# Optimization experiments

Hardware: AMD Instinct MI355X
Metric: run time of the kernel (lower is better)

The kernel has to match this reference:

```python
import jax, jax.numpy as jnp
import numpy as np
from jax import lax

NMS_RADIUS = 4
THRESHOLD = 0.005
BORDER = 4
MAX_KP = 1024


def _max_pool(x, r):
    # torch max_pool2d pads with -inf; reduce_window 'SAME' pads with init value.
    w = 2 * r + 1
    return lax.reduce_window(x, -jnp.inf, lax.max, (1, w, w), (1, 1, 1), 'SAME')


def simple_nms(scores, radius):
    zeros = jnp.zeros_like(scores)
    max_mask = scores == _max_pool(scores, radius)
    for _ in range(2):
        supp_mask = _max_pool(max_mask.astype(scores.dtype), radius) > 0
        supp_scores = jnp.where(supp_mask, zeros, scores)
        new_max_mask = supp_scores == _max_pool(supp_scores, radius)
        max_mask = max_mask | (new_max_mask & ~supp_mask)
    return jnp.where(max_mask, scores, zeros)


def sample_descriptors(kp, desc, s):
    """Bilinear grid_sample (align_corners=True, zero padding) + L2 normalize.
    kp: [B,N,2] (x,y) full-resolution pixel coords; desc: [B,C,h,w]."""
    b, c, h, w = desc.shape
    k = kp - s / 2 + 0.5
    gx = k[..., 0] / (w * s - 1) * 2.0 - 1.0
    gy = k[..., 1] / (h * s - 1) * 2.0 - 1.0
    x = (gx + 1.0) * 0.5 * (w - 1)  # align_corners=True mapping
    y = (gy + 1.0) * 0.5 * (h - 1)
    x0 = jnp.floor(x); y0 = jnp.floor(y)
    wx1 = x - x0; wy1 = y - y0
    x0i = x0.astype(jnp.int32); y0i = y0.astype(jnp.int32)

    def tap(d_b, xi, yi):  # d_b [C,h,w]; xi,yi [N] -> [C,N], zero outside
        v = ((xi >= 0) & (xi < w) & (yi >= 0) & (yi < h)).astype(d_b.dtype)
        g = d_b[:, jnp.clip(yi, 0, h - 1), jnp.clip(xi, 0, w - 1)]
        return g * v

    def one(d_b, x0i, y0i, wx1, wy1):
        wx0 = 1.0 - wx1; wy0 = 1.0 - wy1
        return (tap(d_b, x0i, y0i) * (wx0 * wy0)
                + tap(d_b, x0i + 1, y0i) * (wx1 * wy0)
                + tap(d_b, x0i, y0i + 1) * (wx0 * wy1)
                + tap(d_b, x0i + 1, y0i + 1) * (wx1 * wy1))

    out = jax.vmap(one)(desc, x0i, y0i, wx1, wy1)  # [B,C,N]
    n = jnp.maximum(jnp.linalg.norm(out, axis=1, keepdims=True), 1e-12)
    return out / n


def conv1x1(w, b, x):  # Conv1d kernel_size=1: [O,I] @ [B,I,N]
    return jnp.einsum('oi,bin->bon', w, x) + b[None, :, None]


def setup_inputs() -> dict:
    key = jax.random.key(0)
    ks = jax.random.split(key, 13)
    B, H, W = 4, 480, 640
    inp = {
        'scores': jax.random.uniform(ks[0], (B, H, W), jnp.float32),
        'd1': jax.random.normal(ks[1], (B, 64, H // 2, W // 2), jnp.float32),
        'd2': jax.random.normal(ks[2], (B, 128, H // 4, W // 4), jnp.float32),
        'cDa': jax.random.normal(ks[3], (B, 256, H // 8, W // 8), jnp.float32),
        'd4': jax.random.normal(ks[4], (B, 256, H // 16, W // 16), jnp.float32),
        'lin0_w': jax.random.normal(ks[5], (256, 256), jnp.float32) / np.sqrt(256),
        'lin0_b': jax.random.normal(ks[6], (256,), jnp.float32) * 0.01,
        'lin1_w': jax.random.normal(ks[7], (128, 128), jnp.float32) / np.sqrt(128),
        'lin1_b': jax.random.normal(ks[8], (128,), jnp.float32) * 0.01,
        'lin2_w': jax.random.normal(ks[9], (64, 64), jnp.float32) / np.sqrt(64),
        'lin2_b': jax.random.normal(ks[10], (64,), jnp.float32) * 0.01,
        'merge_w': jax.random.normal(ks[11], (256, 704), jnp.float32) / np.sqrt(704),
        'merge_b': jax.random.normal(ks[12], (256,), jnp.float32) * 0.01,
    }
    return inp


def reference(scores, d1, d2, cDa, d4, lin0_w, lin0_b, lin1_w, lin1_b,
              lin2_w, lin2_b, merge_w, merge_b):
    B, H, W = scores.shape
    s = simple_nms(scores, NMS_RADIUS)
    ys, xs = jnp.meshgrid(jnp.arange(H), jnp.arange(W), indexing='ij')
    valid = (ys >= BORDER) & (ys < H - BORDER) & (xs >= BORDER) & (xs < W - BORDER)
    masked = jnp.where(valid[None] & (s > THRESHOLD), s, -1.0)
    top_scores, idx = lax.top_k(masked.reshape(B, -1), MAX_KP)
    kx = (idx % W).astype(jnp.float32)
    ky = (idx // W).astype(jnp.float32)
    kp = jnp.stack([kx, ky], axis=-1)  # [B,K,2] (x,y), i.e. torch.flip(k,[1])
    de1 = sample_descriptors(kp, d1, 2)    # [B,64,K]
    de2 = sample_descriptors(kp, d2, 4)    # [B,128,K]
    de3 = sample_descriptors(kp, cDa, 8)   # [B,256,K]
    de4 = sample_descriptors(kp, d4, 16)   # [B,256,K]
    de4 = conv1x1(lin0_w, lin0_b, de4)
    de2 = conv1x1(lin1_w, lin1_b, de2)
    de1 = conv1x1(lin2_w, lin2_b, de1)
    descriptors = conv1x1(merge_w, merge_b,
                          jnp.concatenate([de1, de2, de3, de4], axis=1))
    return kp, top_scores, descriptors
```

## Files before the change

### kernel.cpp

```cpp
#include <hip/hip_runtime.h>
#include <hip/hip_bf16.h>

#define B 4
#define H 480
#define W 640
#define HW (H*W)
#define BHW (B*H*W)
#define NKP 1024
#define THRESH 0.005f
#define CAP 16384
#define NCOL (B*NKP)
#define KTOT 704

typedef __attribute__((ext_vector_type(8))) short s8v;
typedef __attribute__((ext_vector_type(4))) float f4v;
typedef struct { float x, y; } __attribute__((aligned(4))) f2u;

__device__ __forceinline__ short f2bf(float f) {
    __hip_bfloat16 h = __float2bfloat16(f);
    return *(short*)&h;
}

__device__ __forceinline__ float max3f(float a, float b, float c) {
    return fmaxf(fmaxf(a, b), c);
}
#define MAX9(A, base, str) \
    max3f(max3f((A)[(base)], (A)[(base)+(str)], (A)[(base)+2*(str)]), \
          max3f((A)[(base)+3*(str)], (A)[(base)+4*(str)], (A)[(base)+5*(str)]), \
          max3f((A)[(base)+6*(str)], (A)[(base)+7*(str)], (A)[(base)+8*(str)]))

__global__ __launch_bounds__(256) void fuse_w(const float* __restrict__ merge_w,
                                              const float* __restrict__ lin0_w,
                                              const float* __restrict__ lin1_w,
                                              const float* __restrict__ lin2_w,
                                              short* __restrict__ Mw) {
    __shared__ float red[4][64];
    int lane = threadIdx.x & 63;
    int wv = threadIdx.x >> 6;
    int jb = blockIdx.x;
    int o = blockIdx.y;
    int j = jb * 64 + lane;
    const float* mwr = merge_w + (size_t)o * KTOT;

    if (jb >= 3 && jb <= 6) {
        if (wv == 0) Mw[(size_t)o * KTOT + j] = f2bf(mwr[j]);
        return;
    }
    float acc = 0.0f;
    if (jb == 0) {
        int k0 = wv * 16;
        #pragma unroll
        for (int k = 0; k < 16; ++k)
            acc += mwr[k0 + k] * lin2_w[(k0 + k) * 64 + lane];
    } else if (jb <= 2) {
        int jj = (jb - 1) * 64 + lane;
        int k0 = wv * 32;
        #pragma unroll
        for (int k = 0; k < 32; ++k)
            acc += mwr[64 + k0 + k] * lin1_w[(k0 + k) * 128 + jj];
    } else {
        int jj = (jb - 7) * 64 + lane;
        int k0 = wv * 64;
        #pragma unroll
        for (int k = 0; k < 64; ++k)
            acc += mwr[448 + k0 + k] * lin0_w[(k0 + k) * 256 + jj];
    }
    red[wv][lane] = acc;
    __syncthreads();
    if (wv == 0) {
        float t = red[0][lane] + red[1][lane] + red[2][lane] + red[3][lane];
        Mw[(size_t)o * KTOT + j] = f2bf(t);
    }
}

__global__ __launch_bounds__(256) void fuse_bias(const float* __restrict__ merge_w,
                                                 const float* __restrict__ merge_b,
                                                 const float* __restrict__ lin0_b,
                                                 const float* __restrict__ lin1_b,
                                                 const float* __restrict__ lin2_b,
                                                 float* __restrict__ biasf,
                                                 int* __restrict__ cnt) {
    int lane = threadIdx.x & 63;
    int wv = threadIdx.x >> 6;
    int o = blockIdx.x * 4 + wv;
    if (blockIdx.x == 0 && threadIdx.x < 4) cnt[threadIdx.x * 64] = 0;
    const float* mwr = merge_w + (size_t)o * KTOT;
    float acc = 0.0f;
    #pragma unroll
    for (int i = 0; i < 11; ++i) {
        int k = i * 64 + lane;
        float c;
        if (k < 64) c = lin2_b[k];
        else if (k < 192) c = lin1_b[k - 64];
        else if (k < 448) c = 0.0f;
        else c = lin0_b[k - 448];
        acc += mwr[k] * c;
    }
    #pragma unroll
    for (int off = 32; off > 0; off >>= 1) acc += __shfl_xor(acc, off, 64);
    if (lane == 0) biasf[o] = merge_b[o] + acc;
}

__global__ __launch_bounds__(256) void transpose_d4(const float* __restrict__ d4,
                                                    float* __restrict__ d4T) {
    __shared__ float T[64][65];
    int b = blockIdx.z;
    int p0 = blockIdx.x * 64;
    int c0 = blockIdx.y * 64;
    for (int t = threadIdx.x; t < 4096; t += 256) {
        int ch = t >> 6, px = t & 63;
        int gp = p0 + px;
        if (gp < 1200)
            T[ch][px] = d4[((size_t)(b * 256 + c0 + ch)) * 1200 + gp];
    }
    __syncthreads();
    for (int t = threadIdx.x; t < 4096; t += 256) {
        int px = t >> 6, ch = t & 63;
        int gp = p0 + px;
        if (gp < 1200)
            d4T[((size_t)(b * 1200 + gp)) * 256 + c0 + ch] = T[ch][px];
    }
}

__global__ __launch_bounds__(256) void transpose_cDa(const float* __restrict__ cDa,
                                                     float* __restrict__ cDaT) {
    __shared__ float T[64][65];
    int b = blockIdx.z;
    int p0 = blockIdx.x * 64;
    int c0 = blockIdx.y * 64;
    for (int t = threadIdx.x; t < 4096; t += 256) {
        int ch = t >> 6, px = t & 63;
        T[ch][px] = cDa[((size_t)(b * 256 + c0 + ch)) * 4800 + p0 + px];
    }
    __syncthreads();
    for (int t = threadIdx.x; t < 4096; t += 256) {
        int px = t >> 6, ch = t & 63;
        cDaT[((size_t)(b * 4800 + p0 + px)) * 256 + c0 + ch] = T[ch][px];
    }
}

__global__ __launch_bounds__(512) void nms_fused(const float* __restrict__ scores,
                                                 unsigned long long* __restrict__ cand,
                                                 int* __restrict__ cnt) {
    __shared__ float S72[72 * 72];
    __shared__ float T72[72 * 64];
    __shared__ float Mm[64 * 64];
    __shared__ float Zm[56 * 56];
    __shared__ int lcnt, gbase;
    int bz = blockIdx.z;
    int x0 = blockIdx.x * 32, y0 = blockIdx.y * 32;
    const float* sp = scores + bz * HW;
    if (threadIdx.x == 0) lcnt = 0;
    for (int t = threadIdx.x; t < 5184; t += 512) {
        int i = t / 72, j = t - i * 72;
        int gy = y0 - 20 + i, gx = x0 - 20 + j;
        S72[t] = (gy >= 0 && gy < H && gx >= 0 && gx < W) ? sp[gy * W + gx] : -1.0f;
    }
    __syncthreads();
    for (int t = threadIdx.x; t < 4608; t += 512) {
        int i = t >> 6, c = t & 63;
        T72[i * 64 + c] = MAX9(S72, i * 72 + c, 1);
    }
    __syncthreads();
    for (int t = threadIdx.x; t < 4096; t += 512) {
        int r = t >> 6, c = t & 63;
        float m = MAX9(T72, r * 64 + c, 64);
        float s = S72[(r + 4) * 72 + c + 4];
        int gy = y0 - 16 + r, gx = x0 - 16 + c;
        Mm[t] = (gy >= 0 && gy < H && gx >= 0 && gx < W && s == m) ? 1.0f : 0.0f;
    }
    __syncthreads();
    float* Tm = T72;
    for (int t = threadIdx.x; t < 3584; t += 512) {
        int i = t / 56, c = t - i * 56;
        Tm[i * 56 + c] = MAX9(Mm, i * 64 + c, 1);
    }
    __syncthreads();
    for (int t = threadIdx.x; t < 3136; t += 512) {
        int i = t / 56, j = t - i * 56;
        float m = MAX9(Tm, i * 56 + j, 56);
        Zm[t] = (m > 0.0f) ? -1.0f : S72[(i + 8) * 72 + (j + 8)];
    }
    __syncthreads();
    for (int t = threadIdx.x; t < 2688; t += 512) {
        int i = t / 48, c = t - i * 48;
        Tm[i * 56 + c] = MAX9(Zm, i * 56 + c, 1);
    }
    __syncthreads();
    for (int t = threadIdx.x; t < 2304; t += 512) {
        int r = t / 48, c = t - r * 48;
        float m = MAX9(Tm, r * 56 + c, 56);
        float Zc = Zm[(r + 4) * 56 + c + 4];
        int mi = (r + 8) * 64 + c + 8;
        bool nm = (Zc == m) && (Zc >= 0.0f);
        Mm[mi] = (Mm[mi] != 0.0f || nm) ? 1.0f : 0.0f;
    }
    __syncthreads();
    for (int t = threadIdx.x; t < 1920; t += 512) {
        int r = t / 40, c = t - r * 40;
        Tm[r * 56 + c] = MAX9(Mm, (r + 8) * 64 + c + 8, 1);
    }
    __syncthreads();
    for (int t = threadIdx.x; t < 1600; t += 512) {
        int r = t / 40, c = t - r * 40;
        float m = MAX9(Tm, r * 56 + c, 56);
        int zi = (r + 8) * 56 + c + 8;
        Zm[zi] = (m > 0.0f) ? -1.0f : S72[(r + 16) * 72 + (c + 16)];
    }
    __syncthreads();
    for (int t = threadIdx.x; t < 1280; t += 512) {
        int r = t / 32, c = t & 31;
        Tm[r * 56 + c] = MAX9(Zm, (r + 8) * 56 + c + 8, 1);
    }
    __syncthreads();
    unsigned long long keys[2];
    int nl = 0;
    #pragma unroll
    for (int q = 0; q < 2; ++q) {
        int t = threadIdx.x + q * 512;
        int r3 = t >> 5, c = t & 31;
        float m = MAX9(Tm, r3 * 56 + c, 56);
        float Zc = Zm[(r3 + 12) * 56 + c + 12];
        bool fin = (Mm[(r3 + 16) * 64 + c + 16] != 0.0f) || ((Zc == m) && (Zc >= 0.0f));
        int gy = y0 + r3, gx = x0 + c;
        float sc = S72[(r3 + 20) * 72 + (c + 20)];
        if (fin && gy >= 4 && gy < H - 4 && gx >= 4 && gx < W - 4 && sc > THRESH) {
            unsigned r = (unsigned)(gy * W + gx);
            unsigned bits = __float_as_uint(sc) | 0x80000000u;
            keys[nl++] = ((unsigned long long)bits << 32) |
                         (unsigned long long)(0xFFFFFFFFu - r);
        }
    }
    int lpos = 0;
    if (nl) lpos = atomicAdd(&lcnt, nl);
    __syncthreads();
    if (threadIdx.x == 0) gbase = (lcnt > 0) ? atomicAdd(&cnt[bz * 64], lcnt) : 0;
    __syncthreads();
    for (int j = 0; j < nl; ++j) {
        int p = gbase + lpos + j;
        if (p < CAP) cand[(size_t)bz * CAP + p] = keys[j];
    }
}

__global__ __launch_bounds__(1024) void topk(const unsigned long long* __restrict__ cand,
                                             const int* __restrict__ cnt,
                                             float* __restrict__ out, int* __restrict__ fidx,
                                             int* __restrict__ perm) {
    __shared__ int hist[2048];
    __shared__ unsigned long long buf[4096];
    __shared__ int scnt, spiv1, spiv2, sabove;
    int b = blockIdx.x, tid = threadIdx.x;
    int m = cnt[b * 64]; if (m > CAP) m = CAP;
    const unsigned long long* cb = cand + (size_t)b * CAP;
    int target = (m < 1024) ? m : 1024;

    hist[tid] = 0; hist[tid + 1024] = 0;
    if (tid == 0) { scnt = 0; spiv1 = 2048; spiv2 = 0; sabove = 0; }
    __syncthreads();
    for (int i = tid; i < m; i += 1024)
        atomicAdd(&hist[(int)(cb[i] >> 53) & 0x7FF], 1);
    __syncthreads();
    for (int d = 1; d < 2048; d <<= 1) {
        int v0 = hist[tid] + ((tid + d < 2048) ? hist[tid + d] : 0);
        int v1 = hist[tid + 1024] + ((tid + 1024 + d < 2048) ? hist[tid + 1024 + d] : 0);
        __syncthreads();
        hist[tid] = v0; hist[tid + 1024] = v1;
        __syncthreads();
    }
    if (target > 0) {
        for (int t = tid; t < 2048; t += 1024) {
            int c = hist[t];
            int cn = (t < 2047) ? hist[t + 1] : 0;
            if (c >= target && cn < target) { spiv1 = t; sabove = cn; }
        }
    }
    __syncthreads();
    int piv1 = spiv1;
    int target2 = target - sabove;
    hist[tid] = 0; hist[tid + 1024] = 0;
    __syncthreads();
    for (int i = tid; i < m; i += 1024) {
        unsigned long long k = cb[i];
        if (((int)(k >> 53) & 0x7FF) == piv1)
            atomicAdd(&hist[(int)(k >> 42) & 0x7FF], 1);
    }
    __syncthreads();
    for (int d = 1; d < 2048; d <<= 1) {
        int v0 = hist[tid] + ((tid + d < 2048) ? hist[tid + d] : 0);
        int v1 = hist[tid + 1024] + ((tid + 1024 + d < 2048) ? hist[tid + 1024 + d] : 0);
        __syncthreads();
        hist[tid] = v0; hist[tid + 1024] = v1;
        __syncthreads();
    }
    if (target > 0) {
        for (int t = tid; t < 2048; t += 1024) {
            int c = hist[t];
            int cn = (t < 2047) ? hist[t + 1] : 0;
            if (c >= target2 && cn < target2) spiv2 = t;
        }
    }
    __syncthreads();
    int piv2 = spiv2;
    for (int i = tid; i < m; i += 1024) {
        unsigned long long k = cb[i];
        int b1 = (int)(k >> 53) & 0x7FF;
        bool sel = (target > 0) &&
                   (b1 > piv1 || (b1 == piv1 && (((int)(k >> 42) & 0x7FF) >= piv2)));
        if (sel) {
            int p = atomicAdd(&scnt, 1);
            if (p < 4096) buf[p] = k;
        }
    }
    __syncthreads();
    int sc_ = scnt; if (sc_ > 4096) sc_ = 4096;
    int ns = 1024; while (ns < sc_) ns <<= 1;
    for (int t = tid; t < ns; t += 1024) if (t >= sc_) buf[t] = 0ULL;
    __syncthreads();
    for (int k = 2; k <= ns; k <<= 1)
        for (int j = k >> 1; j > 0; j >>= 1) {
            __syncthreads();
            for (int t = tid; t < ns; t += 1024) {
                int ixj = t ^ j;
                if (ixj > t) {
                    unsigned long long a = buf[t], bb = buf[ixj];
                    if (((t & k) == 0) ? (a < bb) : (a > bb)) { buf[t] = bb; buf[ixj] = a; }
                }
            }
        }
    __syncthreads();
    unsigned long long key = buf[tid];
    float kx, ky, sc;
    unsigned idx;
    if (key != 0ULL) {
        unsigned ord = (unsigned)(key >> 32);
        sc = __uint_as_float(ord ^ 0x80000000u);
        idx = 0xFFFFFFFFu - (unsigned)(key & 0xFFFFFFFFu);
        kx = (float)(idx % W);
        ky = (float)(idx / W);
    } else {
        sc = -1.0f; idx = 0; kx = 0.0f; ky = 0.0f;
    }
    int bn = b * NKP + tid;
    out[bn * 2 + 0] = kx;
    out[bn * 2 + 1] = ky;
    out[B * NKP * 2 + bn] = sc;
    fidx[bn] = (int)idx;
    __syncthreads();
    if (tid < 512) { hist[tid] = 0; hist[tid + 1024] = 0; }
    __syncthreads();
    int bucket = (int)(idx >> 10);
    atomicAdd(&hist[bucket], 1);
    __syncthreads();
    if (tid < 512) hist[512 + tid] = hist[tid];
    __syncthreads();
    for (int d = 1; d < 512; d <<= 1) {
        int v = 0;
        if (tid < 512) v = hist[512 + tid] + ((tid >= d) ? hist[512 + tid - d] : 0);
        __syncthreads();
        if (tid < 512) hist[512 + tid] = v;
        __syncthreads();
    }
    int intra = atomicAdd(&hist[1024 + bucket], 1);
    int pos = hist[512 + bucket] - hist[bucket] + intra;
    perm[b * NKP + pos] = tid;
}

__global__ __launch_bounds__(256) void sample_all(const float* __restrict__ d1,
                                                  const float* __restrict__ d2,
                                                  const float* __restrict__ cDa,
                                                  const float* __restrict__ d4T,
                                                  const float* __restrict__ cDaT,
                                                  const int* __restrict__ fidx,
                                                  const int* __restrict__ perm,
                                                  short* __restrict__ X) {
    int lane = threadIdx.x & 63;
    int wv = threadIdx.x >> 6;
    int seg = blockIdx.y;
    int bid = blockIdx.x;
    int swz = ((bid & 7) << 7) | (bid >> 3);
    int b = swz >> 8;
    int g0 = ((swz & 255) << 2) + wv;

    const float* map; int h, w, s, C, base, nset;
    if (seg == 0)      { map = d1;  h = 240; w = 320; s = 2;  C = 64;  base = 0;   nset = 1; }
    else if (seg == 1) { map = d2;  h = 120; w = 160; s = 4;  C = 128; base = 64;  nset = 2; }
    else if (seg == 2) { map = cDa; h = 60;  w = 80;  s = 8;  C = 256; base = 192; nset = 4; }
    else               { map = d4T; h = 30;  w = 40;  s = 16; C = 256; base = 448; nset = 4; }

    int col = (b << 10) | perm[(b << 10) + g0];
    int idx = fidx[col];
    float kx = (float)(idx % W);
    float ky = (float)(idx / W);
    float kxs = kx - (float)s * 0.5f + 0.5f;
    float kys = ky - (float)s * 0.5f + 0.5f;
    float gx = kxs / (float)(w * s - 1) * 2.0f - 1.0f;
    float gy = kys / (float)(h * s - 1) * 2.0f - 1.0f;
    float x = (gx + 1.0f) * 0.5f * (float)(w - 1);
    float y = (gy + 1.0f) * 0.5f * (float)(h - 1);
    float x0f = floorf(x), y0f = floorf(y);
    int x0 = (int)x0f, y0 = (int)y0f;
    float wx1 = x - x0f, wy1 = y - y0f;
    float wx0 = 1.0f - wx1, wy0 = 1.0f - wy1;
    bool vx0 = (x0 >= 0) && (x0 < w);
    bool vx1 = (x0 + 1 >= 0) && (x0 + 1 < w);
    bool vy0 = (y0 >= 0) && (y0 < h);
    bool vy1 = (y0 + 1 >= 0) && (y0 + 1 < h);
    int xc0 = min(max(x0, 0), w - 1), xc1 = min(max(x0 + 1, 0), w - 1);
    int yc0 = min(max(y0, 0), h - 1), yc1 = min(max(y0 + 1, 0), h - 1);
    float w00 = (vx0 && vy0) ? wx0 * wy0 : 0.0f;
    float w01 = (vx1 && vy0) ? wx1 * wy0 : 0.0f;
    float w10 = (vx0 && vy1) ? wx0 * wy1 : 0.0f;
    float w11 = (vx1 && vy1) ? wx1 * wy1 : 0.0f;

    bool nhwc = (seg == 3) || (seg == 2 && cDaT != nullptr);
    float vals[4];
    float r = 0.0f;
    if (nhwc) {
        const float* pt;
        int wq;
        if (seg == 3) { pt = d4T + ((size_t)b * 1200) * 256 + lane; wq = 40; }
        else          { pt = cDaT + ((size_t)b * 4800) * 256 + lane; wq = 80; }
        size_t o00 = ((size_t)(yc0 * wq + xc0)) << 8;
        size_t o01 = ((size_t)(yc0 * wq + xc1)) << 8;
        size_t o10 = ((size_t)(yc1 * wq + xc0)) << 8;
        size_t o11 = ((size_t)(yc1 * wq + xc1)) << 8;
        float q00[4], q01[4], q10[4], q11[4];
        #pragma unroll
        for (int j = 0; j < 4; ++j) {
            q00[j] = pt[o00 + j * 64]; q01[j] = pt[o01 + j * 64];
            q10[j] = pt[o10 + j * 64]; q11[j] = pt[o11 + j * 64];
        }
        #pragma unroll
        for (int j = 0; j < 4; ++j) {
            vals[j] = q00[j] * w00 + q01[j] * w01 + q10[j] * w10 + q11[j] * w11;
            r += vals[j] * vals[j];
        }
    } else {
        int xb = min(xc0, w - 2);
        float s0 = (xc0 == xb) ? 1.0f : 0.0f;
        float s1 = (xc1 == xb) ? 1.0f : 0.0f;
        float ax = w00 * s0 + w01 * s1;
        float ay = w00 * (1.0f - s0) + w01 * (1.0f - s1);
        float bx = w10 * s0 + w11 * s1;
        float by = w10 * (1.0f - s0) + w11 * (1.0f - s1);
        size_t hw = (size_t)(h * w);
        const float* pb = map + ((size_t)b * C + lane) * hw;
        size_t off0 = (size_t)yc0 * w + xb;
        size_t off1 = (size_t)yc1 * w + xb;
        size_t cstr = hw << 6;
        f2u q0[4], q1[4];
        #pragma unroll
        for (int j = 0; j < 4; ++j) {
            if (j < nset) {
                const float* p = pb + (size_t)j * cstr;
                q0[j] = *(const f2u*)(p + off0);
                q1[j] = *(const f2u*)(p + off1);
            }
        }
        #pragma unroll
        for (int j = 0; j < 4; ++j) {
            if (j < nset) {
                vals[j] = q0[j].x * ax + q0[j].y * ay + q1[j].x * bx + q1[j].y * by;
                r += vals[j] * vals[j];
            }
        }
    }
    #pragma unroll
    for (int off = 32; off > 0; off >>= 1) r += __shfl_xor(r, off, 64);
    float denom = fmaxf(sqrtf(r), 1e-12f);
    float inv = 1.0f / denom;
    short* xp = X + (size_t)col * KTOT + base + lane;
    #pragma unroll
    for (int j = 0; j < 4; ++j) {
        if (j < nset) xp[j * 64] = f2bf(vals[j] * inv);
    }
}

__global__ __launch_bounds__(256) void gemm_mfma(const short* __restrict__ Mw,
                                                 const short* __restrict__ X,
                                                 const float* __restrict__ biasf,
                                                 float* __restrict__ out) {
    __shared__ short As[64 * 72];
    __shared__ short Bs[64 * 72];
    int tid = threadIdx.x;
    int lane = tid & 63, w = tid >> 6;
    int r = lane & 15, quad = lane >> 4;
    int rowBase = blockIdx.y * 64, colBase = blockIdx.x * 64;
    int sm = tid >> 2, skq = (tid & 3) << 4;

    const short* pa = Mw + (size_t)(rowBase + sm) * KTOT + skq;
    const short* pb = X + (size_t)(colBase + sm) * KTOT + skq;
    s8v a0 = *(const s8v*)(pa), a1 = *(const s8v*)(pa + 8);
    s8v b0 = *(const s8v*)(pb), b1 = *(const s8v*)(pb + 8);

    f4v acc[4];
    #pragma unroll
    for (int t = 0; t < 4; ++t) acc[t] = (f4v)0.0f;

    for (int kt = 0; kt < 11; ++kt) {
        __syncthreads();
        *(s8v*)&As[sm * 72 + skq + 0] = a0;
        *(s8v*)&As[sm * 72 + skq + 8] = a1;
        *(s8v*)&Bs[sm * 72 + skq + 0] = b0;
        *(s8v*)&Bs[sm * 72 + skq + 8] = b1;
        __syncthreads();
        if (kt < 10) {
            pa += 64; pb += 64;
            a0 = *(const s8v*)(pa); a1 = *(const s8v*)(pa + 8);
            b0 = *(const s8v*)(pb); b1 = *(const s8v*)(pb + 8);
        }
        #pragma unroll
        for (int kk = 0; kk < 2; ++kk) {
            int aoff = (w * 16 + r) * 72 + kk * 32 + quad * 8;
            s8v af = *(const s8v*)&As[aoff];
            #pragma unroll
            for (int t = 0; t < 4; ++t) {
                int boff = (t * 16 + r) * 72 + kk * 32 + quad * 8;
                s8v bf = *(const s8v*)&Bs[boff];
                acc[t] = __builtin_amdgcn_mfma_f32_16x16x32_bf16(af, bf, acc[t], 0, 0, 0);
            }
        }
    }
    #pragma unroll
    for (int t = 0; t < 4; ++t) {
        int colg = colBase + t * 16 + r;
        size_t obase = (size_t)(colg >> 10) * (256 * NKP) + (size_t)(colg & 1023);
        #pragma unroll
        for (int reg = 0; reg < 4; ++reg) {
            int row = rowBase + w * 16 + quad * 4 + reg;
            out[obase + (size_t)row * NKP] = acc[t][reg] + biasf[row];
        }
    }
}

extern "C" void kernel_launch(void* const* d_in, const int* in_sizes, int n_in,
                              void* d_out, int out_size, void* d_ws, size_t ws_size,
                              hipStream_t stream) {
    const float* scores  = (const float*)d_in[0];
    const float* d1      = (const float*)d_in[1];
    const float* d2      = (const float*)d_in[2];
    const float* cDa     = (const float*)d_in[3];
    const float* d4      = (const float*)d_in[4];
    const float* lin0_w  = (const float*)d_in[5];
    const float* lin0_b  = (const float*)d_in[6];
    const float* lin1_w  = (const float*)d_in[7];
    const float* lin1_b  = (const float*)d_in[8];
    const float* lin2_w  = (const float*)d_in[9];
    const float* lin2_b  = (const float*)d_in[10];
    const float* merge_w = (const float*)d_in[11];
    const float* merge_b = (const float*)d_in[12];
    float* out = (float*)d_out;

    char* ws = (char*)d_ws;
    short* Xbuf = (short*)ws;
    float* d4T  = (float*)(ws + 6291456);
    unsigned long long* cand  = (unsigned long long*)(ws + 14745600);
    int* cnt                  = (int*)(ws + 15269888);
    int* fidx                 = (int*)(ws + 15401984);
    short* Mw                 = (short*)(ws + 15418368);
    float* biasf              = (float*)(ws + 16139264);
    int* perm                 = (int*)(ws + 16140288);
    float* cDaT = nullptr;
    if (ws_size >= 16156672ULL + 19660800ULL)
        cDaT = (float*)(ws + 16156672);

    dim3 tgrid(W / 32, H / 32, B);

    fuse_w<<<dim3(11, 256), 256, 0, stream>>>(merge_w, lin0_w, lin1_w, lin2_w, Mw);
    fuse_bias<<<64, 256, 0, stream>>>(merge_w, merge_b, lin0_b, lin1_b, lin2_b, biasf, cnt);
    transpose_d4<<<dim3(19, 4, 4), 256, 0, stream>>>(d4, d4T);
    if (cDaT)
        transpose_cDa<<<dim3(75, 4, 4), 256, 0, stream>>>(cDa, cDaT);
    nms_fused<<<tgrid, 512, 0, stream>>>(scores, cand, cnt);
    topk<<<B, 1024, 0, stream>>>(cand, cnt, out, fidx, perm);
    sample_all<<<dim3(1024, 4), 256, 0, stream>>>(d1, d2, cDa, d4T, cDaT, fidx, perm, Xbuf);
    gemm_mfma<<<dim3(NCOL / 64, 256 / 64), 256, 0, stream>>>(Mw, Xbuf, biasf, out + B * NKP * 3);
}
```

Baseline: 310.3 us.

## Use wavefront shuffles for histogram scans and intra-wave bitonic sort stages in topk

Replaces the shared-memory Hillis-Steele suffix scans over the 2048-bin histograms with a two-level wave-shuffle scan plus a small cross-wave carry pass. The bitonic sort now runs every stride below 64 in registers with __shfl_xor, and only strides of 64 and above use shared memory and barriers. The final 512-bucket prefix scan also moves to shuffles. The aim is to cut the many __syncthreads barriers and LDS round trips in the single-block-per-batch topk kernel, at the cost of more complex index and direction logic.

```diff
diff --git a/kernel.cpp b/kernel.cpp
--- a/kernel.cpp
+++ b/kernel.cpp
@@ -247,9 +247,11 @@
                                              float* __restrict__ out, int* __restrict__ fidx,
                                              int* __restrict__ perm) {
     __shared__ int hist[2048];
+    __shared__ int wtot[16], wcarry[16];
     __shared__ unsigned long long buf[4096];
     __shared__ int scnt, spiv1, spiv2, sabove;
     int b = blockIdx.x, tid = threadIdx.x;
+    int lane = tid & 63, wv = tid >> 6;
     int m = cnt[b * 64]; if (m > CAP) m = CAP;
     const unsigned long long* cb = cand + (size_t)b * CAP;
     int target = (m < 1024) ? m : 1024;
@@ -260,13 +262,37 @@
     for (int i = tid; i < m; i += 1024)
         atomicAdd(&hist[(int)(cb[i] >> 53) & 0x7FF], 1);
     __syncthreads();
-    for (int d = 1; d < 2048; d <<= 1) {
-        int v0 = hist[tid] + ((tid + d < 2048) ? hist[tid + d] : 0);
-        int v1 = hist[tid + 1024] + ((tid + 1024 + d < 2048) ? hist[tid + 1024 + d] : 0);
+    {
+        int base = wv * 128;
+        int a = hist[base + lane];
+        int c = hist[base + 64 + lane];
+        int as = a, cs = c;
+        #pragma unroll
+        for (int off = 1; off < 64; off <<= 1) {
+            int t1 = __shfl_down(as, off, 64);
+            if (lane + off < 64) as += t1;
+            int t2 = __shfl_down(cs, off, 64);
+            if (lane + off < 64) cs += t2;
+        }
+        int ctot = __shfl(cs, 0, 64);
+        as += ctot;
+        if (lane == 0) wtot[wv] = as;
         __syncthreads();
-        hist[tid] = v0; hist[tid + 1024] = v1;
+        if (wv == 0 && lane < 16) {
+            int v = wtot[lane];
+            #pragma unroll
+            for (int off = 1; off < 16; off <<= 1) {
+                int t1 = __shfl_down(v, off, 64);
+                if (lane + off < 16) v += t1;
+            }
+            wcarry[lane] = v - wtot[lane];
+        }
         __syncthreads();
-    }
+        int carry = wcarry[wv];
+        hist[base + lane] = as + carry;
+        hist[base + 64 + lane] = cs + carry;
+    }
+    __syncthreads();
     if (target > 0) {
         for (int t = tid; t < 2048; t += 1024) {
             int c = hist[t];
@@ -285,13 +311,37 @@
             atomicAdd(&hist[(int)(k >> 42) & 0x7FF], 1);
     }
     __syncthreads();
-    for (int d = 1; d < 2048; d <<= 1) {
-        int v0 = hist[tid] + ((tid + d < 2048) ? hist[tid + d] : 0);
-        int v1 = hist[tid + 1024] + ((tid + 1024 + d < 2048) ? hist[tid + 1024 + d] : 0);
+    {
+        int base = wv * 128;
+        int a = hist[base + lane];
+        int c = hist[base + 64 + lane];
+        int as = a, cs = c;
+        #pragma unroll
+        for (int off = 1; off < 64; off <<= 1) {
+            int t1 = __shfl_down(as, off, 64);
+            if (lane + off < 64) as += t1;
+            int t2 = __shfl_down(cs, off, 64);
+            if (lane + off < 64) cs += t2;
+        }
+        int ctot = __shfl(cs, 0, 64);
+        as += ctot;
+        if (lane == 0) wtot[wv] = as;
         __syncthreads();
-        hist[tid] = v0; hist[tid + 1024] = v1;
+        if (wv == 0 && lane < 16) {
+            int v = wtot[lane];
+            #pragma unroll
+            for (int off = 1; off < 16; off <<= 1) {
+                int t1 = __shfl_down(v, off, 64);
+                if (lane + off < 16) v += t1;
+            }
+            wcarry[lane] = v - wtot[lane];
+        }
         __syncthreads();
-    }
+        int carry = wcarry[wv];
+        hist[base + lane] = as + carry;
+        hist[base + 64 + lane] = cs + carry;
+    }
+    __syncthreads();
     if (target > 0) {
         for (int t = tid; t < 2048; t += 1024) {
             int c = hist[t];
@@ -316,8 +366,25 @@
     int ns = 1024; while (ns < sc_) ns <<= 1;
     for (int t = tid; t < ns; t += 1024) if (t >= sc_) buf[t] = 0ULL;
     __syncthreads();
-    for (int k = 2; k <= ns; k <<= 1)
-        for (int j = k >> 1; j > 0; j >>= 1) {
+    int nseg = ns >> 6;
+    for (int seg = wv; seg < nseg; seg += 16) {
+        int e = (seg << 6) + lane;
+        unsigned long long v = buf[e];
+        #pragma unroll
+        for (int k = 2; k <= 64; k <<= 1) {
+            #pragma unroll
+            for (int j = k >> 1; j >= 1; j >>= 1) {
+                unsigned long long p = __shfl_xor(v, j, 64);
+                bool upper = (lane & j) != 0;
+                bool dird = ((e & k) == 0);
+                bool keepmax = (dird != upper);
+                v = keepmax ? (v > p ? v : p) : (v < p ? v : p);
+            }
+        }
+        buf[e] = v;
+    }
+    for (int k = 128; k <= ns; k <<= 1) {
+        for (int j = k >> 1; j >= 64; j >>= 1) {
             __syncthreads();
             for (int t = tid; t < ns; t += 1024) {
                 int ixj = t ^ j;
@@ -327,6 +394,21 @@
                 }
             }
         }
+        __syncthreads();
+        for (int seg = wv; seg < nseg; seg += 16) {
+            int e = (seg << 6) + lane;
+            unsigned long long v = buf[e];
+            #pragma unroll
+            for (int j = 32; j >= 1; j >>= 1) {
+                unsigned long long p = __shfl_xor(v, j, 64);
+                bool upper = (lane & j) != 0;
+                bool dird = ((e & k) == 0);
+                bool keepmax = (dird != upper);
+                v = keepmax ? (v > p ? v : p) : (v < p ? v : p);
+            }
+            buf[e] = v;
+        }
+    }
     __syncthreads();
     unsigned long long key = buf[tid];
     float kx, ky, sc;
@@ -351,15 +433,29 @@
     int bucket = (int)(idx >> 10);
     atomicAdd(&hist[bucket], 1);
     __syncthreads();
-    if (tid < 512) hist[512 + tid] = hist[tid];
-    __syncthreads();
-    for (int d = 1; d < 512; d <<= 1) {
-        int v = 0;
-        if (tid < 512) v = hist[512 + tid] + ((tid >= d) ? hist[512 + tid - d] : 0);
-        __syncthreads();
-        if (tid < 512) hist[512 + tid] = v;
-        __syncthreads();
-    }
+    int iv = 0;
+    if (wv < 8) {
+        iv = hist[wv * 64 + lane];
+        #pragma unroll
+        for (int off = 1; off < 64; off <<= 1) {
+            int t1 = __shfl_up(iv, off, 64);
+            if (lane >= off) iv += t1;
+        }
+        if (lane == 63) wtot[wv] = iv;
+    }
+    __syncthreads();
+    if (wv == 0 && lane < 8) {
+        int v = wtot[lane], iv2 = v;
+        #pragma unroll
+        for (int off = 1; off < 8; off <<= 1) {
+            int t1 = __shfl_up(iv2, off, 64);
+            if (lane >= off) iv2 += t1;
+        }
+        wcarry[lane] = iv2 - v;
+    }
+    __syncthreads();
+    if (wv < 8) hist[512 + wv * 64 + lane] = iv + wcarry[wv];
+    __syncthreads();
     int intra = atomicAdd(&hist[1024 + bucket], 1);
     int pos = hist[512 + bucket] - hist[bucket] + intra;
     perm[b * NKP + pos] = tid;
```

New measurement: 296.6 us (median of 2 runs). -4.4%, faster.
